# Kernel tuning notes

Measured on AMD Instinct MI355X. Metric: run time of the kernel, lower is better.

The kernel has to match this reference:

```python
import jax, jax.numpy as jnp
import numpy as np
from math import sqrt

N_USERS = 60000
N_ITEMS = 40000
D = 64
B = 3
LAYERS = 2
E = 600000
BATCH = 2048
N_NODES = (N_USERS + 1) + (N_ITEMS + 1)
REG_WEIGHT = 1e-3
BPR_GAMMA = 1e-10


def setup_inputs() -> dict:
    key = jax.random.key(0)
    k0, k1, k2, k3, k4 = jax.random.split(key, 5)
    user_emb = jax.random.normal(k0, (N_USERS + 1, D), jnp.float32) * 0.1
    item_emb = jax.random.normal(k1, (N_ITEMS + 1, D), jnp.float32) * 0.1
    W = jnp.ones((B,), jnp.float32)
    edge_users = jax.random.randint(k2, (B, E), 1, N_USERS + 1)
    edge_items = jax.random.randint(k3, (B, E), 1, N_ITEMS + 1)
    batch_data = jax.random.randint(k4, (BATCH, B, 3), 1, N_ITEMS + 1)
    return dict(user_emb=user_emb, item_emb=item_emb, W=W,
                edge_users=edge_users, edge_items=edge_items,
                batch_data=batch_data)


def _lightgcn(emb, eu, ei, layers):
    # bipartite undirected graph: users <-> items (items offset by N_USERS+1)
    it = ei + (N_USERS + 1)
    src = jnp.concatenate([eu, it])
    dst = jnp.concatenate([it, eu])
    deg = jax.ops.segment_sum(jnp.ones_like(src, jnp.float32), src, N_NODES)
    norm = jax.lax.rsqrt(jnp.maximum(deg[src], 1.0)) * jax.lax.rsqrt(jnp.maximum(deg[dst], 1.0))
    out = emb
    cur = emb
    for _ in range(layers):
        cur = jax.ops.segment_sum(cur[src] * norm[:, None], dst, N_NODES)
        out = out + cur
    return out / (layers + 1)


def _mutual_attention(f):
    # f: [N, B, D]
    S = jnp.einsum('nid,njd->nij', f, f)          # [N, B, B] pairwise scores
    last = S[:, B - 1:B, :]                        # [N, 1, B]
    proj = S[:, :B - 1, :]                         # [N, B-1, B]
    # (last * proj) * last / (last^2 + eps)   (dim-1 is size 1, sums/norms trivial)
    clear = (last * proj) * last / (last * last + 1e-12)   # [N, B-1, B]
    scores = jnp.sum(clear, axis=1, keepdims=True) + last   # [N, 1, B]
    all_scores = jnp.concatenate([clear, scores], axis=1)   # [N, B, B]
    att = jax.nn.softmax(all_scores / sqrt(D), axis=-1)
    return jnp.einsum('nij,njd->nid', att, f)


def reference(user_emb, item_emb, W, edge_users, edge_items, batch_data):
    total0 = jnp.concatenate([user_emb, item_emb], axis=0)   # [N_NODES, D]
    # global graph = union of all behaviors
    g_eu = edge_users.reshape(-1)
    g_ei = edge_items.reshape(-1)
    all_emb = _lightgcn(total0, g_eu, g_ei, LAYERS)
    # per-behavior propagation
    u_list, i_list = [], []
    for b in range(B):
        eb = _lightgcn(all_emb, edge_users[b], edge_items[b], LAYERS)
        u_list.append(eb[:N_USERS + 1])
        i_list.append(eb[N_USERS + 1:])
    all_user = jnp.stack(u_list, axis=1)   # [n_users+1, B, D]
    all_item = jnp.stack(i_list, axis=1)   # [n_items+1, B, D]
    all_user = _mutual_attention(all_user)
    # item behaviour degree: interactions per item per behavior
    ones = jnp.ones((E,), jnp.float32)
    ibd = jnp.stack([jax.ops.segment_sum(ones, edge_items[b], N_ITEMS + 1)
                     for b in range(B)], axis=1)   # [n_items+1, B]
    weight = ibd * W
    weight = weight / (jnp.sum(weight, axis=1, keepdims=True) + 1e-8)
    item_final = jnp.sum(all_item * weight[:, :, None], axis=1)   # [n_items+1, D]
    total_loss = jnp.float32(0.0)
    for b in range(B):
        users = batch_data[:, b, 0]
        items = batch_data[:, b, 1:3]
        uf = all_user[:, b][users][:, None, :]      # [batch, 1, D]
        itf = item_final[items]                      # [batch, 2, D]
        scores = jnp.sum(uf * itf, axis=2)           # [batch, 2]
        total_loss = total_loss - jnp.mean(
            jnp.log(BPR_GAMMA + jax.nn.sigmoid(scores[:, 0] - scores[:, 1])))
    emb_loss = (jnp.linalg.norm(user_emb) + jnp.linalg.norm(item_emb)) / (N_ITEMS + 1)
    return total_loss + REG_WEIGHT * emb_loss
```

## Files before the change

kernel.cpp:

```cpp
#include <hip/hip_runtime.h>
#include <hip/hip_bf16.h>
#include <math.h>

#define NUQ 60001
#define NIQ 40001
#define NNQ 100002
#define DQ  64
#define EQ  600000
#define BQ  3
#define BATCHQ 2048
#define ROWW 32
#define NSLOT (BATCHQ * BQ)
#define NPAD 100004
#define ADJB 1200000
#define BLK_ELE 2048
#define NBLK ((NNQ + BLK_ELE - 1) / BLK_ELE)
#define RANGE 392
#define NRANGE 256
#define NBINS (BQ * NRANGE)
#define NBLKA 256
#define EPB ((BQ * EQ + NBLKA - 1) / NBLKA)

typedef float f32x2 __attribute__((ext_vector_type(2)));

__device__ __forceinline__ float wave_sum(float v) {
#pragma unroll
  for (int m = 32; m >= 1; m >>= 1) v += __shfl_xor(v, m, 64);
  return v;
}
__device__ __forceinline__ int wave_sum_i(int v) {
#pragma unroll
  for (int m = 32; m >= 1; m >>= 1) v += __shfl_xor(v, m, 64);
  return v;
}

__device__ __forceinline__ unsigned pack_bf2(float lo, float hi) {
  unsigned a = __float_as_uint(lo);
  unsigned b = __float_as_uint(hi);
  a = (a + 0x7FFFu + ((a >> 16) & 1u)) >> 16;
  b = (b + 0x7FFFu + ((b >> 16) & 1u)) >> 16;
  return a | (b << 16);
}
__device__ __forceinline__ float unpk_lo(unsigned u) { return __uint_as_float(u << 16); }
__device__ __forceinline__ float unpk_hi(unsigned u) { return __uint_as_float(u & 0xFFFF0000u); }

__device__ __forceinline__ void ntst_u32(unsigned* p, unsigned v) { __builtin_nontemporal_store(v, p); }

__global__ void zero_i_k(int* __restrict__ p, int n) {
  int tid = blockIdx.x * blockDim.x + threadIdx.x;
  int stride = gridDim.x * blockDim.x;
  for (int i = tid; i < n; i += stride) p[i] = 0;
}

__global__ void binc_k(const int* __restrict__ eu, const int* __restrict__ ei,
                       unsigned* __restrict__ counts) {
  __shared__ unsigned h[NBINS];
  for (int i = threadIdx.x; i < NBINS; i += 256) h[i] = 0u;
  __syncthreads();
  int base = blockIdx.x * EPB;
  int end = base + EPB;
  if (end > BQ * EQ) end = BQ * EQ;
  for (int idx = base + threadIdx.x; idx < end; idx += 256) {
    int b = idx / EQ;
    int u = eu[idx];
    int it = ei[idx] + NUQ;
    atomicAdd(&h[b * NRANGE + u / RANGE], 1u);
    atomicAdd(&h[b * NRANGE + it / RANGE], 1u);
  }
  __syncthreads();
  for (int i = threadIdx.x; i < NBINS; i += 256)
    counts[(size_t)blockIdx.x * NBINS + i] = h[i];
}

__global__ void binscan1_k(const unsigned* __restrict__ counts,
                           unsigned* __restrict__ offs, unsigned* __restrict__ bintot) {
  int bin = blockIdx.x;
  int t = threadIdx.x;
  int lane = t & 63, wid = t >> 6;
  unsigned v = counts[(size_t)t * NBINS + bin];
  unsigned incl = v;
#pragma unroll
  for (int off = 1; off < 64; off <<= 1) {
    unsigned x = __shfl_up(incl, off, 64);
    if (lane >= off) incl += x;
  }
  __shared__ unsigned wsum[4];
  if (lane == 63) wsum[wid] = incl;
  __syncthreads();
  if (t == 0) {
    unsigned s = 0;
#pragma unroll
    for (int w = 0; w < 4; ++w) { unsigned x = wsum[w]; wsum[w] = s; s += x; }
  }
  __syncthreads();
  unsigned excl = incl - v + wsum[wid];
  offs[(size_t)t * NBINS + bin] = excl;
  if (t == 255) bintot[bin] = excl + v;
}

__global__ void binscan2_k(const unsigned* __restrict__ bintot,
                           unsigned* __restrict__ binstart) {
  int t = threadIdx.x;
  int lane = t & 63, wid = t >> 6;
  unsigned c0 = bintot[t * 3 + 0], c1 = bintot[t * 3 + 1], c2 = bintot[t * 3 + 2];
  unsigned tsum = c0 + c1 + c2;
  unsigned incl = tsum;
#pragma unroll
  for (int off = 1; off < 64; off <<= 1) {
    unsigned x = __shfl_up(incl, off, 64);
    if (lane >= off) incl += x;
  }
  __shared__ unsigned wsum[4];
  if (lane == 63) wsum[wid] = incl;
  __syncthreads();
  if (t == 0) {
    unsigned s = 0;
#pragma unroll
    for (int w = 0; w < 4; ++w) { unsigned x = wsum[w]; wsum[w] = s; s += x; }
  }
  __syncthreads();
  unsigned run = incl - tsum + wsum[wid];
  binstart[t * 3 + 0] = run; run += c0;
  binstart[t * 3 + 1] = run; run += c1;
  binstart[t * 3 + 2] = run; run += c2;
  if (t == 255) binstart[NBINS] = run;
}

__global__ void binfill_k(const int* __restrict__ eu, const int* __restrict__ ei,
                          const unsigned* __restrict__ offs,
                          const unsigned* __restrict__ binstart,
                          unsigned* __restrict__ records) {
  __shared__ unsigned cur[NBINS];
  for (int i = threadIdx.x; i < NBINS; i += 256)
    cur[i] = binstart[i] + offs[(size_t)blockIdx.x * NBINS + i];
  __syncthreads();
  int base = blockIdx.x * EPB;
  int end = base + EPB;
  if (end > BQ * EQ) end = BQ * EQ;
  for (int idx = base + threadIdx.x; idx < end; idx += 256) {
    int b = idx / EQ;
    int u = eu[idx];
    int itl = ei[idx];
    int it = itl + NUQ;
    unsigned p = atomicAdd(&cur[b * NRANGE + u / RANGE], 1u);
    records[p] = ((unsigned)(u % RANGE) << 16) | (unsigned)itl;
    unsigned q = atomicAdd(&cur[b * NRANGE + it / RANGE], 1u);
    records[q] = ((unsigned)(it % RANGE) << 16) | (unsigned)u;
  }
}

__global__ void bindeg_k(const unsigned* __restrict__ records,
                         const unsigned* __restrict__ binstart,
                         int* __restrict__ degB) {
  int bin = blockIdx.x;
  int b = bin / NRANGE;
  int r0 = (bin % NRANGE) * RANGE;
  __shared__ int h[RANGE];
  for (int i = threadIdx.x; i < RANGE; i += 256) h[i] = 0;
  __syncthreads();
  unsigned rs = binstart[bin], re = binstart[bin + 1];
  for (unsigned j = rs + threadIdx.x; j < re; j += 256)
    atomicAdd(&h[records[j] >> 16], 1);
  __syncthreads();
  int nval = NNQ - r0;
  if (nval > RANGE) nval = RANGE;
  int* deg = degB + (size_t)b * NPAD;
  for (int i = threadIdx.x; i < nval; i += 256) deg[r0 + i] = h[i];
}

__global__ void scan_p1_k(const int* __restrict__ degB, int* __restrict__ partial) {
  int b = blockIdx.x / NBLK;
  int blk = blockIdx.x % NBLK;
  const int* deg = degB + (size_t)b * NPAD;
  int base = blk * BLK_ELE + threadIdx.x * 8;
  int s = 0;
#pragma unroll
  for (int i = 0; i < 8; ++i) { int idx = base + i; if (idx < NNQ) s += deg[idx]; }
  s = wave_sum_i(s);
  __shared__ int lds[4];
  int wid = threadIdx.x >> 6;
  if ((threadIdx.x & 63) == 0) lds[wid] = s;
  __syncthreads();
  if (threadIdx.x == 0) partial[b * NBLK + blk] = lds[0] + lds[1] + lds[2] + lds[3];
}

__global__ void scan_p2_k(int* __restrict__ partial, int* __restrict__ rowptrB) {
  int wid = threadIdx.x >> 6;
  int lane = threadIdx.x & 63;
  if (wid >= BQ) return;
  int v = (lane < NBLK) ? partial[wid * NBLK + lane] : 0;
  int orig = v;
#pragma unroll
  for (int off = 1; off < 64; off <<= 1) {
    int t = __shfl_up(v, off, 64);
    if (lane >= off) v += t;
  }
  if (lane < NBLK) partial[wid * NBLK + lane] = v - orig;
  if (lane == NBLK - 1) rowptrB[(size_t)wid * NPAD + NNQ] = v;
}

__global__ void scan_p3_k(const int* __restrict__ degB, const int* __restrict__ partial,
                          int* __restrict__ rowptrB, float* __restrict__ invsqB) {
  int b = blockIdx.x / NBLK;
  int blk = blockIdx.x % NBLK;
  const int* deg = degB + (size_t)b * NPAD;
  int* rowptr = rowptrB + (size_t)b * NPAD;
  float* invsq = invsqB + (size_t)b * NPAD;
  int base = blk * BLK_ELE + threadIdx.x * 8;
  int d[8];
  int tsum = 0;
#pragma unroll
  for (int i = 0; i < 8; ++i) {
    int idx = base + i;
    d[i] = (idx < NNQ) ? deg[idx] : 0;
    tsum += d[i];
  }
  int lane = threadIdx.x & 63;
  int wid = threadIdx.x >> 6;
  int incl = tsum;
#pragma unroll
  for (int off = 1; off < 64; off <<= 1) {
    int t = __shfl_up(incl, off, 64);
    if (lane >= off) incl += t;
  }
  int excl = incl - tsum;
  __shared__ int lds[4];
  if (lane == 63) lds[wid] = incl;
  __syncthreads();
  if (threadIdx.x == 0) {
    int s = 0;
#pragma unroll
    for (int w = 0; w < 4; ++w) { int t = lds[w]; lds[w] = s; s += t; }
  }
  __syncthreads();
  int run = excl + lds[wid] + partial[b * NBLK + blk];
#pragma unroll
  for (int i = 0; i < 8; ++i) {
    int idx = base + i;
    if (idx < NNQ) {
      rowptr[idx] = run;
      run += d[i];
      invsq[idx] = rsqrtf(fmaxf((float)d[i], 1.f));
    }
  }
}

__global__ void invsqg_k(const int* __restrict__ degB, float* __restrict__ invsqG) {
  int n = blockIdx.x * blockDim.x + threadIdx.x;
  if (n >= NNQ) return;
  int dg = degB[n] + degB[NPAD + n] + degB[2 * NPAD + n];
  invsqG[n] = rsqrtf(fmaxf((float)dg, 1.f));
}

__global__ void binscat_k(const unsigned* __restrict__ records,
                          const unsigned* __restrict__ binstart,
                          const int* __restrict__ rowptrB,
                          unsigned short* __restrict__ adjB) {
  int bin = blockIdx.x;
  int b = bin / NRANGE;
  int r0 = (bin % NRANGE) * RANGE;
  int nval = NNQ - r0;
  if (nval > RANGE) nval = RANGE;
  __shared__ int cur[RANGE];
  const int* rowptr = rowptrB + (size_t)b * NPAD;
  for (int i = threadIdx.x; i < nval; i += 256) cur[i] = rowptr[r0 + i];
  __syncthreads();
  unsigned rs = binstart[bin], re = binstart[bin + 1];
  unsigned short* adj = adjB + (size_t)b * ADJB;
  for (unsigned j = rs + threadIdx.x; j < re; j += 256) {
    unsigned rec = records[j];
    int dl = rec >> 16;
    int pos = atomicAdd(&cur[dl], 1);
    adj[pos] = (unsigned short)(rec & 0xFFFFu);
  }
}

__global__ void pack_emb_k(const float* __restrict__ ue, const float* __restrict__ ie,
                           unsigned* __restrict__ E0, float* __restrict__ sc) {
  int stride = gridDim.x * blockDim.x;
  float su = 0.f, si = 0.f;
  for (int idx = blockIdx.x * blockDim.x + threadIdx.x; idx < NNQ * ROWW; idx += stride) {
    int n = idx >> 5, k = idx & 31;
    const float* src = (n < NUQ) ? (ue + (size_t)n * DQ) : (ie + (size_t)(n - NUQ) * DQ);
    float a = src[2 * k], b = src[2 * k + 1];
    ntst_u32(&E0[idx], pack_bf2(a, b));
    float v = a * a + b * b;
    if (n < NUQ) su += v; else si += v;
  }
  su = wave_sum(su);
  si = wave_sum(si);
  __shared__ float wsU[4], wsI[4];
  int wid = threadIdx.x >> 6;
  if ((threadIdx.x & 63) == 0) { wsU[wid] = su; wsI[wid] = si; }
  __syncthreads();
  if (threadIdx.x == 0) {
    atomicAdd(sc + 1, wsU[0] + wsU[1] + wsU[2] + wsU[3]);
    atomicAdd(sc + 2, wsI[0] + wsI[1] + wsI[2] + wsI[3]);
  }
}

__device__ __forceinline__ void gather_w32(const unsigned* __restrict__ S,
                                           const unsigned short* __restrict__ adj,
                                           const float* __restrict__ invsq,
                                           int start, int end, int offs,
                                           int l5, int g32, unsigned k4,
                                           float& alo, float& ahi) {
  for (int j0 = start; j0 < end; j0 += 32) {
    int nloc = end - j0;
    if (nloc > 32) nloc = 32;
    unsigned boff = (unsigned)offs << 7;
    float w = 0.f;
    if (l5 < nloc) {
      int a = (int)adj[j0 + l5] + offs;
      boff = (unsigned)a << 7;
      w = invsq[a];
    }
    for (int j = 0; j < nloc; j += 8) {
#pragma unroll
      for (int m = 0; m < 8; ++m) {
        int jj = j + m + g32;
        unsigned bo = (unsigned)__shfl((int)boff, jj, 64) + k4;
        float ww = __shfl(w, jj, 64);
        unsigned dd = *(const unsigned*)((const char*)S + bo);
        alo += ww * unpk_lo(dd);
        ahi += ww * unpk_hi(dd);
      }
    }
  }
}

__device__ __forceinline__ void gather3w32(const unsigned* __restrict__ S,
                                           const unsigned short* __restrict__ adjB,
                                           const float* __restrict__ wtab,
                                           int s0, int d0, int s1, int d1,
                                           int s2, int d2, int offs,
                                           int l5, int g32, unsigned k4,
                                           float& alo, float& ahi) {
  int D = d0 + d1 + d2;
  int d01 = d0 + d1;
  for (int j0 = 0; j0 < D; j0 += 32) {
    int nloc = D - j0;
    if (nloc > 32) nloc = 32;
    unsigned boff = (unsigned)offs << 7;
    float w = 0.f;
    int l = j0 + l5;
    if (l < D) {
      int idx;
      if (l < d0)       idx = s0 + l;
      else if (l < d01) idx = ADJB + s1 + (l - d0);
      else              idx = 2 * ADJB + s2 + (l - d01);
      int a = (int)adjB[idx] + offs;
      boff = (unsigned)a << 7;
      w = wtab[a];
    }
    for (int j = 0; j < nloc; j += 8) {
#pragma unroll
      for (int m = 0; m < 8; ++m) {
        int jj = j + m + g32;
        unsigned bo = (unsigned)__shfl((int)boff, jj, 64) + k4;
        float ww = __shfl(w, jj, 64);
        unsigned dd = *(const unsigned*)((const char*)S + bo);
        alo += ww * unpk_lo(dd);
        ahi += ww * unpk_hi(dd);
      }
    }
  }
}

__device__ __forceinline__ void gather_w64(const unsigned* __restrict__ S,
                                           const unsigned short* __restrict__ adj,
                                           const float* __restrict__ invsq,
                                           int start, int end, int offs,
                                           int lane, unsigned k4, int g,
                                           float& alo, float& ahi) {
  for (int j0 = start; j0 < end; j0 += 64) {
    int nloc = end - j0;
    if (nloc > 64) nloc = 64;
    unsigned boff = (unsigned)offs << 7;
    float w = 0.f;
    if (lane < nloc) {
      int a = (int)adj[j0 + lane] + offs;
      boff = (unsigned)a << 7;
      w = invsq[a];
    }
    for (int j = 0; j < nloc; j += 16) {
#pragma unroll
      for (int m = 0; m < 8; ++m) {
        int jj = j + 2 * m + g;
        unsigned bo = (unsigned)__shfl((int)boff, jj, 64) + k4;
        float ww = __shfl(w, jj, 64);
        unsigned dd = *(const unsigned*)((const char*)S + bo);
        alo += ww * unpk_lo(dd);
        ahi += ww * unpk_hi(dd);
      }
    }
  }
}

__global__ void g_l1_k(const unsigned* __restrict__ E0, unsigned* __restrict__ T1,
                       const int* __restrict__ rowptrB, const unsigned short* __restrict__ adjB,
                       const float* __restrict__ invsqG) {
  int wv = (blockIdx.x * blockDim.x + threadIdx.x) >> 6;
  int lane = threadIdx.x & 63;
  int g = lane >> 5;
  int node = wv * 2 + g;
  if (node >= NNQ) return;
  int l5 = lane & 31, g32 = g << 5;
  unsigned k4 = (unsigned)l5 << 2;
  int offs = (node < NUQ) ? NUQ : 0;
  int s0 = rowptrB[node], d0 = rowptrB[node + 1] - s0;
  int s1 = rowptrB[NPAD + node], d1 = rowptrB[NPAD + node + 1] - s1;
  int s2 = rowptrB[2 * NPAD + node], d2 = rowptrB[2 * NPAD + node + 1] - s2;
  float alo = 0.f, ahi = 0.f;
  gather3w32(E0, adjB, invsqG, s0, d0, s1, d1, s2, d2, offs, l5, g32, k4, alo, ahi);
  float s = invsqG[node];
  ntst_u32(&T1[(size_t)node * ROWW + l5], pack_bf2(alo * s, ahi * s));
}

__global__ void g_l2c_k(const unsigned* __restrict__ E0, const unsigned* __restrict__ T1,
                        unsigned* __restrict__ C,
                        const int* __restrict__ rowptrB, const unsigned short* __restrict__ adjB,
                        const float* __restrict__ invsqG) {
  int wv = (blockIdx.x * blockDim.x + threadIdx.x) >> 6;
  int lane = threadIdx.x & 63;
  int g = lane >> 5;
  int node = wv * 2 + g;
  if (node >= NNQ) return;
  int l5 = lane & 31, g32 = g << 5;
  unsigned k4 = (unsigned)l5 << 2;
  int offs = (node < NUQ) ? NUQ : 0;
  int s0 = rowptrB[node], d0 = rowptrB[node + 1] - s0;
  int s1 = rowptrB[NPAD + node], d1 = rowptrB[NPAD + node + 1] - s1;
  int s2 = rowptrB[2 * NPAD + node], d2 = rowptrB[2 * NPAD + node + 1] - s2;
  float alo = 0.f, ahi = 0.f;
  gather3w32(T1, adjB, invsqG, s0, d0, s1, d1, s2, d2, offs, l5, g32, k4, alo, ahi);
  float s = invsqG[node];
  size_t rb = (size_t)node * ROWW + l5;
  unsigned e0 = E0[rb];
  unsigned t1 = T1[rb];
  float clo = (unpk_lo(e0) + unpk_lo(t1) + alo * s) * (1.f / 3.f);
  float chi = (unpk_hi(e0) + unpk_hi(t1) + ahi * s) * (1.f / 3.f);
  ntst_u32(&C[rb], pack_bf2(clo, chi));
}

__global__ void b_l1_k(const unsigned* __restrict__ C, unsigned* __restrict__ T1B,
                       const int* __restrict__ rowptrB, const unsigned short* __restrict__ adjB,
                       const float* __restrict__ invsqB) {
  int wv = (blockIdx.x * blockDim.x + threadIdx.x) >> 6;
  int lane = threadIdx.x & 63;
  int g = lane >> 5;
  int node = wv * 2 + g;
  if (node >= NNQ) return;
  int b = blockIdx.y;
  const int* rowptr = rowptrB + (size_t)b * NPAD;
  const float* iv = invsqB + (size_t)b * NPAD;
  int l5 = lane & 31, g32 = g << 5;
  unsigned k4 = (unsigned)l5 << 2;
  int offs = (node < NUQ) ? NUQ : 0;
  float alo = 0.f, ahi = 0.f;
  gather_w32(C, adjB + (size_t)b * ADJB, iv, rowptr[node], rowptr[node + 1], offs, l5, g32, k4, alo, ahi);
  float s = iv[node];
  ntst_u32(&T1B[(size_t)b * NNQ * ROWW + (size_t)node * ROWW + l5], pack_bf2(alo * s, ahi * s));
}

__global__ void mega_slot_k(const unsigned* __restrict__ C, const unsigned* __restrict__ T1B,
                            const int* __restrict__ rowptrB, const unsigned short* __restrict__ adjB,
                            const float* __restrict__ invsqB, const int* __restrict__ degB,
                            const int* __restrict__ batch, const float* __restrict__ W,
                            float* __restrict__ acc) {
  int slot = (blockIdx.x * blockDim.x + threadIdx.x) >> 6;
  int lane = threadIdx.x & 63;
  float val = 0.f;
  if (slot < NSLOT) {
    int k = lane & 31, g = lane >> 5;
    unsigned k4 = (unsigned)k << 2;
    int u = batch[slot * 3 + 0];
    f32x2 a0v, a1v, a2v;
#pragma unroll
    for (int b = 0; b < BQ; ++b) {
      const int* rp = rowptrB + (size_t)b * NPAD;
      const float* iv = invsqB + (size_t)b * NPAD;
      const unsigned* T1 = T1B + (size_t)b * NNQ * ROWW;
      float alo = 0.f, ahi = 0.f;
      gather_w64(T1, adjB + (size_t)b * ADJB, iv, rp[u], rp[u + 1], NUQ, lane, k4, g, alo, ahi);
      alo += __shfl_xor(alo, 32, 64);
      ahi += __shfl_xor(ahi, 32, 64);
      float s = iv[u];
      size_t rb = (size_t)u * ROWW + k;
      unsigned c0 = C[rb];
      unsigned t0 = T1[rb];
      f32x2 o;
      o.x = (unpk_lo(c0) + unpk_lo(t0) + alo * s) * (1.f / 3.f);
      o.y = (unpk_hi(c0) + unpk_hi(t0) + ahi * s) * (1.f / 3.f);
      if (b == 0) a0v = o; else if (b == 1) a1v = o; else a2v = o;
    }
    float p00 = 0.5f * wave_sum(a0v.x * a0v.x + a0v.y * a0v.y);
    float p01 = 0.5f * wave_sum(a0v.x * a1v.x + a0v.y * a1v.y);
    float p02 = 0.5f * wave_sum(a0v.x * a2v.x + a0v.y * a2v.y);
    float p11 = 0.5f * wave_sum(a1v.x * a1v.x + a1v.y * a1v.y);
    float p12 = 0.5f * wave_sum(a1v.x * a2v.x + a1v.y * a2v.y);
    float p22 = 0.5f * wave_sum(a2v.x * a2v.x + a2v.y * a2v.y);
    int bb = slot % BQ;
    float last[3] = {p02, p12, p22};
    float S0[3] = {p00, p01, p02};
    float S1[3] = {p01, p11, p12};
    float rows[3][3];
#pragma unroll
    for (int j = 0; j < 3; ++j) {
      float l = last[j];
      float f = l * l / (l * l + 1e-12f);
      float c0 = S0[j] * f;
      float c1 = S1[j] * f;
      rows[0][j] = c0;
      rows[1][j] = c1;
      rows[2][j] = c0 + c1 + l;
    }
    float x0 = rows[bb][0] * 0.125f, x1 = rows[bb][1] * 0.125f, x2 = rows[bb][2] * 0.125f;
    float m = fmaxf(x0, fmaxf(x1, x2));
    float e0 = expf(x0 - m), e1 = expf(x1 - m), e2 = expf(x2 - m);
    float inv = 1.f / (e0 + e1 + e2);
    f32x2 uf;
    uf.x = (e0 * a0v.x + e1 * a1v.x + e2 * a2v.x) * inv;
    uf.y = (e0 * a0v.y + e1 * a1v.y + e2 * a2v.y) * inv;
    float sco[2];
#pragma unroll
    for (int c = 0; c < 2; ++c) {
      int node = batch[slot * 3 + 1 + c] + NUQ;
      f32x2 i0v, i1v, i2v;
#pragma unroll
      for (int b = 0; b < BQ; ++b) {
        const int* rp = rowptrB + (size_t)b * NPAD;
        const float* iv = invsqB + (size_t)b * NPAD;
        const unsigned* T1 = T1B + (size_t)b * NNQ * ROWW;
        float alo = 0.f, ahi = 0.f;
        gather_w64(T1, adjB + (size_t)b * ADJB, iv, rp[node], rp[node + 1], 0, lane, k4, g, alo, ahi);
        alo += __shfl_xor(alo, 32, 64);
        ahi += __shfl_xor(ahi, 32, 64);
        float s = iv[node];
        size_t rb = (size_t)node * ROWW + k;
        unsigned c0 = C[rb];
        unsigned t0 = T1[rb];
        f32x2 o;
        o.x = (unpk_lo(c0) + unpk_lo(t0) + alo * s) * (1.f / 3.f);
        o.y = (unpk_hi(c0) + unpk_hi(t0) + ahi * s) * (1.f / 3.f);
        if (b == 0) i0v = o; else if (b == 1) i1v = o; else i2v = o;
      }
      float w0 = (float)degB[0 * NPAD + node] * W[0];
      float w1 = (float)degB[1 * NPAD + node] * W[1];
      float w2 = (float)degB[2 * NPAD + node] * W[2];
      float inv2 = 1.f / (w0 + w1 + w2 + 1e-8f);
      f32x2 ifv;
      ifv.x = (i0v.x * w0 + i1v.x * w1 + i2v.x * w2) * inv2;
      ifv.y = (i0v.y * w0 + i1v.y * w1 + i2v.y * w2) * inv2;
      sco[c] = 0.5f * wave_sum(uf.x * ifv.x + uf.y * ifv.y);
    }
    if (lane == 0) {
      float x = sco[0] - sco[1];
      float sg = 1.f / (1.f + expf(-x));
      val = -logf(1e-10f + sg) * (1.f / (float)BATCHQ);
    }
  }
  __shared__ float ws[4];
  if (lane == 0) ws[threadIdx.x >> 6] = val;
  __syncthreads();
  if (threadIdx.x == 0) atomicAdd(acc, ws[0] + ws[1] + ws[2] + ws[3]);
}

__global__ void finalize_k(const float* __restrict__ sc, unsigned int* __restrict__ out) {
  float total = sc[0] + 0.001f * (sqrtf(sc[1]) + sqrtf(sc[2])) / (float)NIQ;
  unsigned int bits = __float_as_uint(total);
  unsigned int lsb = (bits >> 16) & 1u;
  unsigned int rb = (bits + 0x7FFFu + lsb) >> 16;
  out[0] = (rb << 16) | rb;
}

extern "C" void kernel_launch(void* const* d_in, const int* in_sizes, int n_in,
                              void* d_out, int out_size, void* d_ws, size_t ws_size,
                              hipStream_t stream) {
  const float* ue = (const float*)d_in[0];
  const float* ie = (const float*)d_in[1];
  const float* W  = (const float*)d_in[2];
  const int* eu    = (const int*)d_in[3];
  const int* ei    = (const int*)d_in[4];
  const int* batch = (const int*)d_in[5];

  unsigned* E0  = (unsigned*)d_ws;
  unsigned* T1  = E0 + (size_t)NNQ * ROWW;
  unsigned* C   = T1 + (size_t)NNQ * ROWW;
  unsigned* T1B = C + (size_t)NNQ * ROWW;
  unsigned short* adjB = (unsigned short*)(T1B + (size_t)BQ * NNQ * ROWW);
  int* rowptrB= (int*)(adjB + (size_t)BQ * ADJB);
  int* degB   = rowptrB + 3 * NPAD;
  float* invsqB = (float*)(degB + 3 * NPAD);
  float* invsqG = invsqB + 3 * NPAD;
  unsigned* counts = (unsigned*)(invsqG + NPAD);
  unsigned* offs   = counts + (size_t)NBLKA * NBINS;
  unsigned* bintot = offs + (size_t)NBLKA * NBINS;
  unsigned* binstart = bintot + 1024;
  unsigned* records = binstart + 1024;
  int* partial  = (int*)(records + (size_t)2 * BQ * EQ);
  float* sc   = (float*)(partial + 256);

  zero_i_k<<<1, 64, 0, stream>>>((int*)sc, 8);

  binc_k<<<NBLKA, 256, 0, stream>>>(eu, ei, counts);
  binscan1_k<<<NBINS, 256, 0, stream>>>(counts, offs, bintot);
  binscan2_k<<<1, 256, 0, stream>>>(bintot, binstart);
  binfill_k<<<NBLKA, 256, 0, stream>>>(eu, ei, offs, binstart, records);
  bindeg_k<<<NBINS, 256, 0, stream>>>(records, binstart, degB);
  scan_p1_k<<<BQ * NBLK, 256, 0, stream>>>(degB, partial);
  scan_p2_k<<<1, 256, 0, stream>>>(partial, rowptrB);
  scan_p3_k<<<BQ * NBLK, 256, 0, stream>>>(degB, partial, rowptrB, invsqB);
  invsqg_k<<<(NNQ + 255) / 256, 256, 0, stream>>>(degB, invsqG);
  binscat_k<<<NBINS, 256, 0, stream>>>(records, binstart, rowptrB, adjB);

  pack_emb_k<<<512, 256, 0, stream>>>(ue, ie, E0, sc);

  const int NODE_BLKS2 = (NNQ / 2 + 4) / 4;

  g_l1_k<<<NODE_BLKS2, 256, 0, stream>>>(E0, T1, rowptrB, adjB, invsqG);
  g_l2c_k<<<NODE_BLKS2, 256, 0, stream>>>(E0, T1, C, rowptrB, adjB, invsqG);

  b_l1_k<<<dim3(NODE_BLKS2, 3), 256, 0, stream>>>(C, T1B, rowptrB, adjB, invsqB);

  mega_slot_k<<<(NSLOT + 3) / 4, 256, 0, stream>>>(C, T1B, rowptrB, adjB, invsqB, degB, batch, W, sc);
  finalize_k<<<1, 1, 0, stream>>>(sc, (unsigned int*)d_out);
}
```

Measured before the change: 401.3 us.

## Fold degree counting into binning pass with global atomics and widen binning grid

Drops the separate bindeg_k pass that re-read the binned records to build per-node degrees. binc_k now increments degB directly with global atomics, and degB is zeroed beforehand. The binning grid grows from 256 to 1024 blocks, so binscan1 now scans four per-block counts per thread. This removes one kernel launch and a full read of the records, at the cost of 3.6M scattered global atomics and a larger counts/offs array to scan.

After: 540.2 us. 1.35x slower.

```diff
diff --git a/kernel.cpp b/kernel.cpp
--- a/kernel.cpp
+++ b/kernel.cpp
@@ -18,7 +18,7 @@
 #define RANGE 392
 #define NRANGE 256
 #define NBINS (BQ * NRANGE)
-#define NBLKA 256
+#define NBLKA 1024
 #define EPB ((BQ * EQ + NBLKA - 1) / NBLKA)
 
 typedef float f32x2 __attribute__((ext_vector_type(2)));
@@ -53,7 +53,7 @@
 }
 
 __global__ void binc_k(const int* __restrict__ eu, const int* __restrict__ ei,
-                       unsigned* __restrict__ counts) {
+                       unsigned* __restrict__ counts, int* __restrict__ degB) {
   __shared__ unsigned h[NBINS];
   for (int i = threadIdx.x; i < NBINS; i += 256) h[i] = 0u;
   __syncthreads();
@@ -66,6 +66,8 @@
     int it = ei[idx] + NUQ;
     atomicAdd(&h[b * NRANGE + u / RANGE], 1u);
     atomicAdd(&h[b * NRANGE + it / RANGE], 1u);
+    atomicAdd(&degB[(size_t)b * NPAD + u], 1);
+    atomicAdd(&degB[(size_t)b * NPAD + it], 1);
   }
   __syncthreads();
   for (int i = threadIdx.x; i < NBINS; i += 256)
@@ -77,8 +79,14 @@
   int bin = blockIdx.x;
   int t = threadIdx.x;
   int lane = t & 63, wid = t >> 6;
-  unsigned v = counts[(size_t)t * NBINS + bin];
-  unsigned incl = v;
+  unsigned v[4];
+  unsigned tsum = 0;
+#pragma unroll
+  for (int i = 0; i < 4; ++i) {
+    v[i] = counts[(size_t)(t * 4 + i) * NBINS + bin];
+    tsum += v[i];
+  }
+  unsigned incl = tsum;
 #pragma unroll
   for (int off = 1; off < 64; off <<= 1) {
     unsigned x = __shfl_up(incl, off, 64);
@@ -93,9 +101,13 @@
     for (int w = 0; w < 4; ++w) { unsigned x = wsum[w]; wsum[w] = s; s += x; }
   }
   __syncthreads();
-  unsigned excl = incl - v + wsum[wid];
-  offs[(size_t)t * NBINS + bin] = excl;
-  if (t == 255) bintot[bin] = excl + v;
+  unsigned run = incl - tsum + wsum[wid];
+#pragma unroll
+  for (int i = 0; i < 4; ++i) {
+    offs[(size_t)(t * 4 + i) * NBINS + bin] = run;
+    run += v[i];
+  }
+  if (t == 255) bintot[bin] = run;
 }
 
 __global__ void binscan2_k(const unsigned* __restrict__ bintot,
@@ -147,25 +159,6 @@
     unsigned q = atomicAdd(&cur[b * NRANGE + it / RANGE], 1u);
     records[q] = ((unsigned)(it % RANGE) << 16) | (unsigned)u;
   }
-}
-
-__global__ void bindeg_k(const unsigned* __restrict__ records,
-                         const unsigned* __restrict__ binstart,
-                         int* __restrict__ degB) {
-  int bin = blockIdx.x;
-  int b = bin / NRANGE;
-  int r0 = (bin % NRANGE) * RANGE;
-  __shared__ int h[RANGE];
-  for (int i = threadIdx.x; i < RANGE; i += 256) h[i] = 0;
-  __syncthreads();
-  unsigned rs = binstart[bin], re = binstart[bin + 1];
-  for (unsigned j = rs + threadIdx.x; j < re; j += 256)
-    atomicAdd(&h[records[j] >> 16], 1);
-  __syncthreads();
-  int nval = NNQ - r0;
-  if (nval > RANGE) nval = RANGE;
-  int* deg = degB + (size_t)b * NPAD;
-  for (int i = threadIdx.x; i < nval; i += 256) deg[r0 + i] = h[i];
 }
 
 __global__ void scan_p1_k(const int* __restrict__ degB, int* __restrict__ partial) {
@@ -602,12 +595,12 @@
   float* sc   = (float*)(partial + 256);
 
   zero_i_k<<<1, 64, 0, stream>>>((int*)sc, 8);
-
-  binc_k<<<NBLKA, 256, 0, stream>>>(eu, ei, counts);
+  zero_i_k<<<512, 256, 0, stream>>>(degB, 3 * NPAD);
+
+  binc_k<<<NBLKA, 256, 0, stream>>>(eu, ei, counts, degB);
   binscan1_k<<<NBINS, 256, 0, stream>>>(counts, offs, bintot);
   binscan2_k<<<1, 256, 0, stream>>>(bintot, binstart);
   binfill_k<<<NBLKA, 256, 0, stream>>>(eu, ei, offs, binstart, records);
-  bindeg_k<<<NBINS, 256, 0, stream>>>(records, binstart, degB);
   scan_p1_k<<<BQ * NBLK, 256, 0, stream>>>(degB, partial);
   scan_p2_k<<<1, 256, 0, stream>>>(partial, rowptrB);
   scan_p3_k<<<BQ * NBLK, 256, 0, stream>>>(degB, partial, rowptrB, invsqB);
```
